# Performance work log

Hardware: AMD Instinct MI355X
Metric: run time of the kernel (lower is better)

The kernel has to match this reference:

```python
import jax, jax.numpy as jnp
import numpy as np

B, C, H, W, O = 8, 128, 256, 256, 128


def setup_inputs() -> dict:
    key = jax.random.key(0)
    k1, k2, k3, k4 = jax.random.split(key, 4)
    x = jax.random.normal(k1, (B, C, H, W), dtype=jnp.float32)
    theta_s = jax.random.uniform(k2, (C, 2), dtype=jnp.float32, minval=-1.0, maxval=1.0)
    w_dw = jax.random.normal(k3, (C,), dtype=jnp.float32) * 0.1   # depthwise 1x1, groups=C
    w_pw = jax.random.normal(k4, (O, C), dtype=jnp.float32) * (1.0 / np.sqrt(C))  # pointwise 1x1
    return {"x": x, "theta_s": theta_s, "w_dw": w_dw, "w_pw": w_pw}


def reference(x, theta_s, w_dw, w_pw):
    b, c, h, w = x.shape
    # zero pad by 1 (ZeroPad2d(1)); shift operates on the padded map, output is interior
    xp = jnp.pad(x, ((0, 0), (0, 0), (1, 1), (1, 1)))
    hp, wp = h + 2, w + 2
    t = -theta_s                      # (C, 2); torch code negates theta
    ft = jnp.floor(t)
    dt = t - ft                       # fractional part, (C, 2)
    ft = ft.astype(jnp.int32)
    # interior grid of the padded map: rows/cols 1..h / 1..w
    m = jnp.arange(1, h + 1)
    n = jnp.arange(1, w + 1)
    y0 = jnp.clip(m[None, :] + ft[:, 0:1], 0, hp - 1)      # (C, h)
    y1 = jnp.clip(m[None, :] + ft[:, 0:1] + 1, 0, hp - 1)  # (C, h)
    x0 = jnp.clip(n[None, :] + ft[:, 1:2], 0, wp - 1)      # (C, w)
    x1 = jnp.clip(n[None, :] + ft[:, 1:2] + 1, 0, wp - 1)  # (C, w)
    cidx = jnp.arange(c)[:, None, None]                    # (C,1,1)
    # gather four bilinear corners for all channels at once -> (B, C, h, w)
    z1 = xp[:, cidx, y0[:, :, None], x0[:, None, :]]
    z2 = xp[:, cidx, y0[:, :, None], x1[:, None, :]]
    z3 = xp[:, cidx, y1[:, :, None], x0[:, None, :]]
    z4 = xp[:, cidx, y1[:, :, None], x1[:, None, :]]
    dy = dt[:, 0][None, :, None, None]
    dx = dt[:, 1][None, :, None, None]
    s = (z1 * (1 - dy) * (1 - dx) + z2 * (1 - dy) * dx
         + z3 * dy * (1 - dx) + z4 * dy * dx)
    # depthwise 1x1 (groups=C): per-channel scale
    s = s * w_dw[None, :, None, None]
    # pointwise 1x1
    return jnp.einsum('bchw,oc->bohw', s, w_pw)
```

## Files before the change

### kernel.cpp

```cpp
#include <hip/hip_runtime.h>

#define B_ 8
#define C_ 128
#define H_ 256
#define W_ 256
#define O_ 128
#define PAD 136
#define WT 128

typedef __bf16 bf16x8 __attribute__((ext_vector_type(8)));
typedef float floatx4 __attribute__((ext_vector_type(4)));

__device__ __forceinline__ float ldpad(const float* __restrict__ xc, int y, int x) {
    bool in = (y >= 1) & (y <= H_) & (x >= 1) & (x <= W_);
    return in ? xc[(y - 1) * W_ + (x - 1)] : 0.0f;
}

__global__ __launch_bounds__(256, 2)
void activeshift_kernel(const float* __restrict__ x,
                        const float* __restrict__ theta,
                        const float* __restrict__ wdw,
                        const float* __restrict__ wpw,
                        float* __restrict__ out)
{
    __shared__ __align__(16) __bf16 w_lds[O_ * PAD];
    __shared__ __align__(16) __bf16 s_lds[WT * PAD];
    __shared__ int4 t_lds[C_];

    const int n  = blockIdx.x;
    const int wt = n & 1;
    const int h  = (n >> 1) & (H_ - 1);
    const int b  = n >> 9;
    const int w0 = wt * WT;
    const int tid = threadIdx.x;

    if (tid < C_) {
        float t0 = -theta[tid * 2 + 0];
        float t1 = -theta[tid * 2 + 1];
        float f0 = floorf(t0), f1 = floorf(t1);
        int4 v;
        v.x = (int)f0;
        v.y = (int)f1;
        v.z = __float_as_int(t0 - f0);
        v.w = __float_as_int(t1 - f1);
        t_lds[tid] = v;
    }

    {
        const float dwv = wdw[tid & (C_ - 1)];
        #pragma unroll
        for (int i = 0; i < 64; ++i) {
            int idx = tid + i * 256;
            int c = idx & (C_ - 1);
            int o = idx >> 7;
            w_lds[o * PAD + c] = (__bf16)(wpw[idx] * dwv);
        }
    }
    __syncthreads();

    const int p    = tid & (WT - 1);
    const int half = tid >> 7;
    const int m  = h + 1;
    const int nn = w0 + p + 1;
    const float* xb = x + (size_t)b * C_ * H_ * W_;

    for (int it = 0; it < 8; ++it) {
        int c0 = it * 16 + half * 8;
        union { bf16x8 v; __bf16 e[8]; } pk;
        #pragma unroll
        for (int cc = 0; cc < 8; ++cc) {
            int c = c0 + cc;
            int4 tv = t_lds[c];
            float dy = __int_as_float(tv.z);
            float dx = __int_as_float(tv.w);
            int y0 = m + tv.x, y1 = y0 + 1;
            int x0 = nn + tv.y, x1 = x0 + 1;
            y0 = min(max(y0, 0), H_ + 1); y1 = min(max(y1, 0), H_ + 1);
            x0 = min(max(x0, 0), W_ + 1); x1 = min(max(x1, 0), W_ + 1);
            const float* xc = xb + (size_t)c * (H_ * W_);
            float v00 = ldpad(xc, y0, x0);
            float v01 = ldpad(xc, y0, x1);
            float v10 = ldpad(xc, y1, x0);
            float v11 = ldpad(xc, y1, x1);
            float r0 = v00 + dx * (v01 - v00);
            float r1 = v10 + dx * (v11 - v10);
            pk.e[cc] = (__bf16)(r0 + dy * (r1 - r0));
        }
        *(bf16x8*)&s_lds[p * PAD + c0] = pk.v;
    }
    __syncthreads();

    const int wid  = tid >> 6;
    const int lane = tid & 63;
    const int wo   = (wid >> 1) * 64;
    const int wp   = (wid & 1) * 64;
    const int l15  = lane & 15;
    const int quad = lane >> 4;

    floatx4 acc[4][4];
    #pragma unroll
    for (int i = 0; i < 4; ++i)
        #pragma unroll
        for (int j = 0; j < 4; ++j)
            acc[i][j] = (floatx4){0.f, 0.f, 0.f, 0.f};

    #pragma unroll
    for (int k = 0; k < C_; k += 32) {
        bf16x8 af[4], bfr[4];
        #pragma unroll
        for (int i = 0; i < 4; ++i)
            af[i] = *(const bf16x8*)&w_lds[(wo + i * 16 + l15) * PAD + k + quad * 8];
        #pragma unroll
        for (int j = 0; j < 4; ++j)
            bfr[j] = *(const bf16x8*)&s_lds[(wp + j * 16 + l15) * PAD + k + quad * 8];
        #pragma unroll
        for (int i = 0; i < 4; ++i)
            #pragma unroll
            for (int j = 0; j < 4; ++j)
                acc[i][j] = __builtin_amdgcn_mfma_f32_16x16x32_bf16(af[i], bfr[j], acc[i][j], 0, 0, 0);
    }

    const size_t HW = (size_t)H_ * W_;
    float* ob = out + (size_t)b * O_ * HW + (size_t)h * W_;
    #pragma unroll
    for (int i = 0; i < 4; ++i) {
        #pragma unroll
        for (int j = 0; j < 4; ++j) {
            int pcol  = w0 + wp + j * 16 + l15;
            int obase = wo + i * 16 + quad * 4;
            float* op = ob + (size_t)obase * HW + pcol;
            #pragma unroll
            for (int r = 0; r < 4; ++r)
                op[(size_t)r * HW] = acc[i][j][r];
        }
    }
}

extern "C" void kernel_launch(void* const* d_in, const int* in_sizes, int n_in,
                              void* d_out, int out_size, void* d_ws, size_t ws_size,
                              hipStream_t stream) {
    const float* x     = (const float*)d_in[0];
    const float* theta = (const float*)d_in[1];
    const float* wdw   = (const float*)d_in[2];
    const float* wpw   = (const float*)d_in[3];
    float* out = (float*)d_out;
    dim3 grid(B_ * H_ * (W_ / WT));
    activeshift_kernel<<<grid, dim3(256), 0, stream>>>(x, theta, wdw, wpw, out);
}
```

Before: 532.8 us.

## Keep pointwise weights in registers and process four rows per block

Weight fragments (pointwise times depthwise, cast to bf16) are now built directly in registers once per block instead of being staged through LDS, and each block loops over 4 output rows, amortising that setup. The activation tile in LDS drops its padding and uses an XOR swizzle to avoid bank conflicts. Occupancy hint is raised to 3 blocks per SM, and boundary handling uses clamped unconditional loads with masks. The costs are higher register pressure from 16 held fragments and fewer blocks in the grid.

Result: slower. 633.3 us (+18.8%).

```diff
diff --git a/kernel.cpp b/kernel.cpp
--- a/kernel.cpp
+++ b/kernel.cpp
@@ -5,34 +5,30 @@
 #define H_ 256
 #define W_ 256
 #define O_ 128
-#define PAD 136
 #define WT 128
+#define RH 4
 
 typedef __bf16 bf16x8 __attribute__((ext_vector_type(8)));
 typedef float floatx4 __attribute__((ext_vector_type(4)));
 
-__device__ __forceinline__ float ldpad(const float* __restrict__ xc, int y, int x) {
-    bool in = (y >= 1) & (y <= H_) & (x >= 1) & (x <= W_);
-    return in ? xc[(y - 1) * W_ + (x - 1)] : 0.0f;
-}
 
-__global__ __launch_bounds__(256, 2)
+__global__ __launch_bounds__(256, 3)
 void activeshift_kernel(const float* __restrict__ x,
                         const float* __restrict__ theta,
                         const float* __restrict__ wdw,
                         const float* __restrict__ wpw,
                         float* __restrict__ out)
 {
-    __shared__ __align__(16) __bf16 w_lds[O_ * PAD];
-    __shared__ __align__(16) __bf16 s_lds[WT * PAD];
+    __shared__ __align__(16) __bf16 s_lds[WT * 128];
     __shared__ int4 t_lds[C_];
 
-    const int n  = blockIdx.x;
-    const int wt = n & 1;
-    const int h  = (n >> 1) & (H_ - 1);
-    const int b  = n >> 9;
-    const int w0 = wt * WT;
-    const int tid = threadIdx.x;
+    const int n     = blockIdx.x;
+    const int strip = n & 1;
+    const int hb    = (n >> 1) & (H_/RH - 1);
+    const int b     = n >> 7;
+    const int w0    = strip * WT;
+    const int h0    = hb * RH;
+    const int tid   = threadIdx.x;
 
     if (tid < C_) {
         float t0 = -theta[tid * 2 + 0];
@@ -46,93 +42,118 @@
         t_lds[tid] = v;
     }
 
-    {
-        const float dwv = wdw[tid & (C_ - 1)];
+    const int wid  = tid >> 6;
+    const int lane = tid & 63;
+    const int wo   = (wid >> 1) * 64;
+    const int wpx  = (wid & 1) * 64;
+    const int l15  = lane & 15;
+    const int quad = lane >> 4;
+
+    bf16x8 afrag[4][4];
+    #pragma unroll
+    for (int ks = 0; ks < 4; ++ks) {
+        int cb = ks * 32 + quad * 8;
+        float4 da = *(const float4*)(wdw + cb);
+        float4 db = *(const float4*)(wdw + cb + 4);
         #pragma unroll
-        for (int i = 0; i < 64; ++i) {
-            int idx = tid + i * 256;
-            int c = idx & (C_ - 1);
-            int o = idx >> 7;
-            w_lds[o * PAD + c] = (__bf16)(wpw[idx] * dwv);
+        for (int i = 0; i < 4; ++i) {
+            int o = wo + i * 16 + l15;
+            float4 wa = *(const float4*)(wpw + o * C_ + cb);
+            float4 wb = *(const float4*)(wpw + o * C_ + cb + 4);
+            bf16x8 f;
+            f[0] = (__bf16)(wa.x * da.x); f[1] = (__bf16)(wa.y * da.y);
+            f[2] = (__bf16)(wa.z * da.z); f[3] = (__bf16)(wa.w * da.w);
+            f[4] = (__bf16)(wb.x * db.x); f[5] = (__bf16)(wb.y * db.y);
+            f[6] = (__bf16)(wb.z * db.z); f[7] = (__bf16)(wb.w * db.w);
+            afrag[ks][i] = f;
         }
     }
-    __syncthreads();
 
     const int p    = tid & (WT - 1);
     const int half = tid >> 7;
-    const int m  = h + 1;
-    const int nn = w0 + p + 1;
-    const float* xb = x + (size_t)b * C_ * H_ * W_;
+    const float* xb = x + (size_t)b * (C_ * H_ * W_);
+    const size_t HW = (size_t)H_ * W_;
 
-    for (int it = 0; it < 8; ++it) {
-        int c0 = it * 16 + half * 8;
-        union { bf16x8 v; __bf16 e[8]; } pk;
-        #pragma unroll
-        for (int cc = 0; cc < 8; ++cc) {
-            int c = c0 + cc;
-            int4 tv = t_lds[c];
-            float dy = __int_as_float(tv.z);
-            float dx = __int_as_float(tv.w);
-            int y0 = m + tv.x, y1 = y0 + 1;
-            int x0 = nn + tv.y, x1 = x0 + 1;
-            y0 = min(max(y0, 0), H_ + 1); y1 = min(max(y1, 0), H_ + 1);
-            x0 = min(max(x0, 0), W_ + 1); x1 = min(max(x1, 0), W_ + 1);
-            const float* xc = xb + (size_t)c * (H_ * W_);
-            float v00 = ldpad(xc, y0, x0);
-            float v01 = ldpad(xc, y0, x1);
-            float v10 = ldpad(xc, y1, x0);
-            float v11 = ldpad(xc, y1, x1);
-            float r0 = v00 + dx * (v01 - v00);
-            float r1 = v10 + dx * (v11 - v10);
-            pk.e[cc] = (__bf16)(r0 + dy * (r1 - r0));
-        }
-        *(bf16x8*)&s_lds[p * PAD + c0] = pk.v;
-    }
     __syncthreads();
 
-    const int wid  = tid >> 6;
-    const int lane = tid & 63;
-    const int wo   = (wid >> 1) * 64;
-    const int wp   = (wid & 1) * 64;
-    const int l15  = lane & 15;
-    const int quad = lane >> 4;
+    for (int hr = 0; hr < RH; ++hr) {
+        const int h = h0 + hr;
 
-    floatx4 acc[4][4];
-    #pragma unroll
-    for (int i = 0; i < 4; ++i)
-        #pragma unroll
-        for (int j = 0; j < 4; ++j)
-            acc[i][j] = (floatx4){0.f, 0.f, 0.f, 0.f};
+        for (int it = 0; it < 8; ++it) {
+            int c0 = it * 16 + half * 8;
+            union { bf16x8 v; __bf16 e[8]; } pk;
+            #pragma unroll
+            for (int cc = 0; cc < 8; ++cc) {
+                int c = c0 + cc;
+                int4 tv = t_lds[c];
+                float dy = __int_as_float(tv.z);
+                float dx = __int_as_float(tv.w);
+                int Y0 = h + tv.x;
+                int X0 = w0 + p + tv.y;
+                int Yc0 = min(max(Y0, 0), H_ - 1);
+                int Yc1 = min(max(Y0 + 1, 0), H_ - 1);
+                int Xc0 = min(max(X0, 0), W_ - 1);
+                int Xc1 = min(max(X0 + 1, 0), W_ - 1);
+                bool ry0 = (unsigned)Y0 < (unsigned)H_;
+                bool ry1 = (unsigned)(Y0 + 1) < (unsigned)H_;
+                bool cx0 = (unsigned)X0 < (unsigned)W_;
+                bool cx1 = (unsigned)(X0 + 1) < (unsigned)W_;
+                const float* cbase = xb + (size_t)c * HW;
+                int r0o = Yc0 * W_, r1o = Yc1 * W_;
+                float v00 = cbase[r0o + Xc0];
+                float v01 = cbase[r0o + Xc1];
+                float v10 = cbase[r1o + Xc0];
+                float v11 = cbase[r1o + Xc1];
+                v00 = (ry0 && cx0) ? v00 : 0.0f;
+                v01 = (ry0 && cx1) ? v01 : 0.0f;
+                v10 = (ry1 && cx0) ? v10 : 0.0f;
+                v11 = (ry1 && cx1) ? v11 : 0.0f;
+                float r0 = v00 + dx * (v01 - v00);
+                float r1 = v10 + dx * (v11 - v10);
+                pk.e[cc] = (__bf16)(r0 + dy * (r1 - r0));
+            }
+            int blk = (it * 2 + half) ^ (p & 7);
+            *(bf16x8*)&s_lds[p * 128 + blk * 8] = pk.v;
+        }
+        __syncthreads();
 
-    #pragma unroll
-    for (int k = 0; k < C_; k += 32) {
-        bf16x8 af[4], bfr[4];
-        #pragma unroll
-        for (int i = 0; i < 4; ++i)
-            af[i] = *(const bf16x8*)&w_lds[(wo + i * 16 + l15) * PAD + k + quad * 8];
-        #pragma unroll
-        for (int j = 0; j < 4; ++j)
-            bfr[j] = *(const bf16x8*)&s_lds[(wp + j * 16 + l15) * PAD + k + quad * 8];
+        floatx4 acc[4][4];
         #pragma unroll
         for (int i = 0; i < 4; ++i)
             #pragma unroll
             for (int j = 0; j < 4; ++j)
-                acc[i][j] = __builtin_amdgcn_mfma_f32_16x16x32_bf16(af[i], bfr[j], acc[i][j], 0, 0, 0);
-    }
+                acc[i][j] = (floatx4){0.f, 0.f, 0.f, 0.f};
 
-    const size_t HW = (size_t)H_ * W_;
-    float* ob = out + (size_t)b * O_ * HW + (size_t)h * W_;
-    #pragma unroll
-    for (int i = 0; i < 4; ++i) {
         #pragma unroll
-        for (int j = 0; j < 4; ++j) {
-            int pcol  = w0 + wp + j * 16 + l15;
-            int obase = wo + i * 16 + quad * 4;
-            float* op = ob + (size_t)obase * HW + pcol;
+        for (int ks = 0; ks < 4; ++ks) {
+            bf16x8 bfr[4];
             #pragma unroll
-            for (int r = 0; r < 4; ++r)
-                op[(size_t)r * HW] = acc[i][j][r];
+            for (int j = 0; j < 4; ++j) {
+                int np = wpx + j * 16 + l15;
+                int blk = (ks * 4 + quad) ^ (np & 7);
+                bfr[j] = *(const bf16x8*)&s_lds[np * 128 + blk * 8];
+            }
+            #pragma unroll
+            for (int i = 0; i < 4; ++i)
+                #pragma unroll
+                for (int j = 0; j < 4; ++j)
+                    acc[i][j] = __builtin_amdgcn_mfma_f32_16x16x32_bf16(afrag[ks][i], bfr[j], acc[i][j], 0, 0, 0);
         }
+
+        float* ob = out + (size_t)b * O_ * HW + (size_t)h * W_;
+        #pragma unroll
+        for (int i = 0; i < 4; ++i) {
+            #pragma unroll
+            for (int j = 0; j < 4; ++j) {
+                int pcol  = w0 + wpx + j * 16 + l15;
+                int obase = wo + i * 16 + quad * 4;
+                float* op = ob + (size_t)obase * HW + pcol;
+                #pragma unroll
+                for (int r = 0; r < 4; ++r)
+                    op[(size_t)r * HW] = acc[i][j][r];
+            }
+        }
+        __syncthreads();
     }
 }
 
@@ -144,6 +165,6 @@
     const float* wdw   = (const float*)d_in[2];
     const float* wpw   = (const float*)d_in[3];
     float* out = (float*)d_out;
-    dim3 grid(B_ * H_ * (W_ / WT));
+    dim3 grid(B_ * (H_ / RH) * (W_ / WT));
     activeshift_kernel<<<grid, dim3(256), 0, stream>>>(x, theta, wdw, wpw, out);
 }
```
